# Optimization experiments

Hardware: AMD Instinct MI355X
Metric: run time of the kernel (lower is better)

The kernel has to match this reference:

```python
import jax, jax.numpy as jnp
import numpy as np

H, L, N1, N2, N3 = 256, 141, 9, 34, 98
B, S = 64, 512

def setup_inputs() -> dict:
    key = jax.random.key(0)
    cnt = [0]
    def nrm(shape, s=0.05):
        cnt[0] += 1
        return jax.random.normal(jax.random.fold_in(key, cnt[0]), shape, jnp.float32) * s
    d = {}
    d['inputs'] = jax.random.randint(jax.random.fold_in(key, 1000), (B, S), 0, 30522)
    d['text_hidden'] = nrm((B, S, 768), 1.0)
    d['label_encoding'] = nrm((L, H), 1.0)
    d['w12'] = (jax.random.uniform(jax.random.fold_in(key, 1001), (N1, N2)) < 0.3).astype(jnp.float32)
    d['w23'] = (jax.random.uniform(jax.random.fold_in(key, 1002), (N2, N3)) < 0.3).astype(jnp.float32)
    d['fre12'] = jax.random.uniform(jax.random.fold_in(key, 1003), (N1, N2), jnp.float32)
    d['fre23'] = jax.random.uniform(jax.random.fold_in(key, 1004), (N2, N3), jnp.float32)
    for name in ['wi1', 'wf1', 'wo1', 'wu1', 'wi2', 'wf2', 'wo2', 'wu2']:
        d[name + '_W'] = nrm((H, H)); d[name + '_b'] = nrm((H,))
    for name in ['ui1', 'uf1', 'uo1', 'uu1', 'ui2', 'uf2', 'uo2', 'uu2']:
        d[name + '_W'] = nrm((H, H))
    d['mix_W'] = nrm((3 * H, H)); d['mix_b'] = nrm((H,))
    d['tt_W'] = nrm((768, H)); d['tt_b'] = nrm((H,))
    d['A'] = nrm((L, L)); d['Wp'] = nrm((H, H))
    d['out_W'] = nrm((L * H, L)); d['out_b'] = nrm((L,))
    return d

def reference(inputs, text_hidden, label_encoding, w12, w23, fre12, fre23,
              wi1_W, wi1_b, wf1_W, wf1_b, wo1_W, wo1_b, wu1_W, wu1_b,
              wi2_W, wi2_b, wf2_W, wf2_b, wo2_W, wo2_b, wu2_W, wu2_b,
              ui1_W, uf1_W, uo1_W, uu1_W, ui2_W, uf2_W, uo2_W, uu2_W,
              mix_W, mix_b, tt_W, tt_b, A, Wp, out_W, out_b):
    sig, tanh = jax.nn.sigmoid, jnp.tanh
    v1 = label_encoding[:N1]          # [N1,H]
    v2 = label_encoding[N1:N1 + N2]   # [N2,H]
    v3 = label_encoding[N1 + N2:]     # [N3,H]
    w21, w32 = w12.T, w23.T
    # --- top-down tree-LSTM (suffix 1) ---
    i11 = sig(v1 @ wi1_W + wi1_b); o11 = sig(v1 @ wo1_W + wo1_b); u11 = tanh(v1 @ wu1_W + wu1_b)
    c11 = i11 * u11; h11 = o11 * tanh(c11)
    h21t = w21 @ h11
    i21 = sig(v2 @ wi1_W + wi1_b + h21t @ ui1_W)
    f21 = sig(v2 @ wf1_W + wf1_b + h21t @ uf1_W)
    o21 = sig(v2 @ wo1_W + wo1_b + h21t @ uo1_W)
    u21 = tanh(v2 @ wu1_W + wu1_b + h21t @ uu1_W)
    c21 = i21 * u21 + f21 * (w21 @ c11); h21 = o21 * tanh(c21)
    h31t = w32 @ h21
    i31 = sig(v3 @ wi1_W + wi1_b + h31t @ ui1_W)
    f31 = sig(v3 @ wf1_W + wf1_b + h31t @ uf1_W)
    o31 = sig(v3 @ wo1_W + wo1_b + h31t @ uo1_W)
    u31 = tanh(v3 @ wu1_W + wu1_b + h31t @ uu1_W)
    c31 = i31 * u31 + f31 * (w32 @ c21); h31 = o31 * tanh(c31)
    # --- bottom-up tree-LSTM (suffix 2) ---
    i32 = sig(v3 @ wi2_W + wi2_b); o32 = sig(v3 @ wo2_W + wo2_b); u32 = tanh(v3 @ wu2_W + wu2_b)
    c32 = i32 * u32; h32 = o32 * tanh(c32)
    h22t = fre23 @ h32
    i22 = sig(v2 @ wi2_W + wi2_b + h22t @ ui2_W)
    f22 = sig((w32 @ v2) @ wf2_W + wf2_b + h32 @ uf2_W)   # [N3,H]
    o22 = sig(v2 @ wo2_W + wo2_b + h22t @ uo2_W)
    u22 = tanh(v2 @ wu2_W + wu2_b + h22t @ uu2_W)
    c22 = i22 * u22 + w23 @ (f22 * c32); h22 = o22 * tanh(c22)
    h12t = fre12 @ h22
    i12 = sig(v1 @ wi2_W + wi2_b + h12t @ ui2_W)
    f12 = sig((w21 @ v1) @ wf2_W + wf2_b + h22 @ uf2_W)   # [N2,H]
    o12 = sig(v1 @ wo2_W + wo2_b + h12t @ uo2_W)
    u12 = tanh(v1 @ wu2_W + wu2_b + h12t @ uu2_W)
    c12 = i12 * u12 + w12 @ (f12 * c22); h12 = o12 * tanh(c12)
    h1 = jnp.concatenate([h11, h12], axis=1)
    h2 = jnp.concatenate([h21, h22], axis=1)
    h3 = jnp.concatenate([h31, h32], axis=1)
    le = jnp.concatenate([h1, h2, h3], axis=0)            # [L,2H]
    temp = jax.nn.relu(A @ label_encoding @ Wp)           # [L,H]
    le = jnp.concatenate([le, temp], axis=1) @ mix_W + mix_b  # [L,H]
    # --- masked cross-attention pooling over text ---
    text = tanh(text_hidden @ tt_W + tt_b)                # [B,S,H]
    att = jnp.einsum('lh,bsh->bls', le, text)             # [B,L,S]
    pad = jnp.where((inputs == 0) | (inputs == 101) | (inputs == 102), -jnp.inf, 0.0).astype(text.dtype)
    att = jax.nn.softmax(att + pad[:, None, :], axis=2)
    features = jnp.einsum('bls,bsh->blh', att, text).reshape(inputs.shape[0], -1)  # [B,L*H]
    return sig(features @ out_W + out_b)                  # [B,L]
```

## Files before the change

kernel.cpp:

```cpp
#include <hip/hip_runtime.h>
#include <math.h>

static constexpr int H = 256, L = 141, N1 = 9, N2 = 34, N3 = 98;
static constexpr int B = 64, S = 512;

typedef __attribute__((ext_vector_type(8))) _Float16 f16x8;
typedef __attribute__((ext_vector_type(4))) float f32x4;

__device__ inline unsigned short f2h(float x) {
    _Float16 h = (_Float16)x;
    return __builtin_bit_cast(unsigned short, h);
}
__device__ inline float sigf(float x) { return 1.f / (1.f + __expf(-x)); }

__device__ inline void gload_lds16(const void* g, void* l) {
    __builtin_amdgcn_global_load_lds(
        (const __attribute__((address_space(1))) void*)g,
        (__attribute__((address_space(3))) void*)l, 16, 0, 0);
}

__global__ __launch_bounds__(256) void conv_ttW(
    const float* __restrict__ W, unsigned short* __restrict__ Bt)
{
    __shared__ unsigned short Tl[32][257];
    const int t = blockIdx.x, tid = threadIdx.x;
    #pragma unroll
    for (int p = 0; p < 32; p++) {
        int lin = p * 256 + tid;
        int r = lin >> 8, c = lin & 255;
        Tl[r][c] = f2h(W[(long)(t * 32 + r) * 256 + c]);
    }
    __syncthreads();
    unsigned short v[32];
    #pragma unroll
    for (int kin = 0; kin < 32; kin++) v[kin] = Tl[kin][tid];
    uint4* dst = (uint4*)(Bt + ((long)t * 256 + tid) * 32);
    #pragma unroll
    for (int q = 0; q < 4; q++) dst[q] = ((const uint4*)v)[q];
}

__global__ __launch_bounds__(512, 4) void text_gemm3(
    const float* __restrict__ Af,
    const unsigned short* __restrict__ Bt,
    const float* __restrict__ bias,
    unsigned short* __restrict__ outH,
    unsigned short* __restrict__ outHT)
{
    __shared__ unsigned short smem[28672];
    unsigned short* As = smem;
    unsigned short* Bs = smem + 4096;
    unsigned short* T  = smem;

    const int tid  = threadIdx.x;
    const int wave = tid >> 6, lane = tid & 63;
    const int quad = lane >> 4, l16 = lane & 15;
    const int m0 = blockIdx.x * 64;
    const int wm = (wave >> 2) * 32;
    const int wn = (wave & 3) * 64;

    const int arow = tid >> 3;
    const int ac16 = tid & 7;
    const float* aSrc = Af + (long)(m0 + arow) * 768 + ac16 * 4;
    const int ac8d = ac16 ^ ((arow & 3) << 1);
    const int aWoff = arow * 32 + ac8d * 4;

    const int bsc = (lane & 3) ^ ((lane >> 3) & 3);
    const long bSrcOff0 = (long)(wave * 32 + (lane >> 2)) * 32 + bsc * 8;
    const long bSrcOff1 = bSrcOff0 + 16 * 32;
    const int bDst0 = (wave * 32) * 32, bDst1 = (wave * 32 + 16) * 32;

    int aro[2], bro[4];
    #pragma unroll
    for (int i = 0; i < 2; i++) {
        int r = wm + i * 16 + l16;
        aro[i] = r * 32 + ((quad * 2) ^ ((r & 3) << 1)) * 4;
    }
    #pragma unroll
    for (int j = 0; j < 4; j++) {
        int n = wn + j * 16 + l16;
        bro[j] = n * 32 + ((quad ^ ((n >> 1) & 3)) << 3);
    }

    f32x4 acc[2][4] = {};
    float4 ar0, ar1;

    auto issueB = [&](int kt, int pb) {
        const unsigned short* src = Bt + (long)kt * 8192;
        unsigned short* d = Bs + pb * 8192;
        gload_lds16(src + bSrcOff0, d + bDst0);
        gload_lds16(src + bSrcOff1, d + bDst1);
    };
    auto writeA = [&](const float4& v, int pa) {
        unsigned int p0 = f2h(v.x) | ((unsigned int)f2h(v.y) << 16);
        unsigned int p1 = f2h(v.z) | ((unsigned int)f2h(v.w) << 16);
        *(uint2*)&As[pa * 2048 + aWoff] = make_uint2(p0, p1);
    };

    ar0 = *(const float4*)(aSrc + 0 * 32);
    issueB(0, 0);
    ar1 = *(const float4*)(aSrc + 1 * 32);
    issueB(1, 1);
    asm volatile("s_waitcnt vmcnt(5)" ::: "memory");
    writeA(ar0, 0);
    asm volatile("s_waitcnt vmcnt(3)" ::: "memory");
    asm volatile("s_waitcnt lgkmcnt(0)" ::: "memory");
    asm volatile("s_barrier" ::: "memory");

    auto body = [&](int t, float4& arIn, float4& arOut, int pa, int pr) {
        int kt2 = (t + 2 <= 23) ? t + 2 : 23;
        arOut = *(const float4*)(aSrc + kt2 * 32);
        f16x8 a[2], b[4];
        const unsigned short* ab = As + pa * 2048;
        const unsigned short* bb = Bs + pr * 8192;
        #pragma unroll
        for (int i = 0; i < 2; i++) a[i] = *(const f16x8*)&ab[aro[i]];
        #pragma unroll
        for (int j = 0; j < 4; j++) b[j] = *(const f16x8*)&bb[bro[j]];
        #pragma unroll
        for (int i = 0; i < 2; i++)
            #pragma unroll
            for (int j = 0; j < 4; j++)
                acc[i][j] = __builtin_amdgcn_mfma_f32_16x16x32_f16(
                    a[i], b[j], acc[i][j], 0, 0, 0);
        asm volatile("s_waitcnt vmcnt(3)" ::: "memory");
        writeA(arIn, pa ^ 1);
        int pw = pr + 2; if (pw >= 3) pw -= 3;
        issueB(kt2, pw);
        asm volatile("s_waitcnt vmcnt(3)" ::: "memory");
        asm volatile("s_waitcnt lgkmcnt(0)" ::: "memory");
        asm volatile("s_barrier" ::: "memory");
    };

    int pr = 0;
    #pragma unroll 1
    for (int t = 0; t < 24; t += 2) {
        body(t,     ar1, ar0, t & 1 ? 1 : 0, pr);
        int pr1 = pr + 1; if (pr1 >= 3) pr1 -= 3;
        body(t + 1, ar0, ar1, 1, pr1);
        pr = pr1 + 1; if (pr >= 3) pr -= 3;
    }
    asm volatile("s_waitcnt vmcnt(0)" ::: "memory");
    __syncthreads();

    float bv[4];
    #pragma unroll
    for (int j = 0; j < 4; j++) bv[j] = bias[wn + j * 16 + l16];

    #pragma unroll
    for (int i = 0; i < 2; i++) {
        #pragma unroll
        for (int j = 0; j < 4; j++) {
            const int mlb = wm + i * 16 + quad * 4;
            const int n   = wn + j * 16 + l16;
            unsigned short hv[4];
            #pragma unroll
            for (int r = 0; r < 4; r++) {
                float v = tanhf(acc[i][j][r] + bv[j]);
                hv[r] = f2h(v);
                outH[(long)(m0 + mlb + r) * 256 + n] = hv[r];
            }
            uint2 p;
            p.x = hv[0] | ((unsigned int)hv[1] << 16);
            p.y = hv[2] | ((unsigned int)hv[3] << 16);
            *(uint2*)&T[n * 72 + mlb] = p;
        }
    }
    __syncthreads();
    {
        const int bb2 = m0 >> 9, s0 = m0 & 511;
        const int n = tid >> 1, half = tid & 1;
        const uint4* src = (const uint4*)&T[n * 72 + half * 32];
        uint4* dst = (uint4*)&outHT[((long)bb2 * 256 + n) * 512 + s0 + half * 32];
        dst[0] = src[0]; dst[1] = src[1];
        dst[2] = src[2]; dst[3] = src[3];
    }
}

__global__ __launch_bounds__(512, 4) void att_logits(
    const unsigned short* __restrict__ le_h,
    const unsigned short* __restrict__ text_h,
    const int* __restrict__ tokens,
    float* __restrict__ att)
{
    __shared__ unsigned short A_s[64 * 256];
    __shared__ unsigned short Bs[3][256 * 32];
    const int tid  = threadIdx.x;
    const int wave = tid >> 6, lane = tid & 63;
    const int quad = lane >> 4, l16 = lane & 15;
    const int s0 = blockIdx.x * 256;
    const int m0 = blockIdx.y * 64;
    const int b  = blockIdx.z;
    const int wm = (wave >> 2) * 32;
    const int wn = (wave & 3) * 64;

    const int bsc = (lane & 3) ^ ((lane >> 3) & 3);
    const long bOff0 = (long)(b * 512 + s0 + wave * 32 + (lane >> 2)) * 256 + bsc * 8;
    const long bOff1 = bOff0 + 16 * 256;
    const int bDst0 = (wave * 32) * 32, bDst1 = bDst0 + 16 * 32;
    auto issueB = [&](int kt, int pb) {
        gload_lds16(text_h + bOff0 + kt * 32, &Bs[pb][bDst0]);
        gload_lds16(text_h + bOff1 + kt * 32, &Bs[pb][bDst1]);
    };

    int abase[2], axm[2], bro[4];
    #pragma unroll
    for (int i = 0; i < 2; i++) {
        int r = wm + i * 16 + l16;
        abase[i] = r * 256; axm[i] = r & 7;
    }
    #pragma unroll
    for (int j = 0; j < 4; j++) {
        int n = wn + j * 16 + l16;
        bro[j] = n * 32 + ((quad ^ ((n >> 1) & 3)) << 3);
    }

    #pragma unroll
    for (int p = 0; p < 4; p++) {
        int row = p * 16 + (tid >> 5);
        int c   = tid & 31;
        int grow = m0 + row; if (grow > L - 1) grow = L - 1;
        gload_lds16(le_h + (long)grow * 256 + ((c ^ (row & 7)) << 3),
                    A_s + p * 4096 + wave * 512);
    }
    issueB(0, 0);
    issueB(1, 1);
    asm volatile("s_waitcnt vmcnt(2)" ::: "memory");
    asm volatile("s_barrier" ::: "memory");

    f32x4 acc[2][4] = {};
    #pragma unroll 1
    for (int t = 0; t < 8; t++) {
        const int pr = t % 3;
        f16x8 a[2], b[4];
        #pragma unroll
        for (int i = 0; i < 2; i++)
            a[i] = *(const f16x8*)&A_s[abase[i] + (((t * 4 + quad) ^ axm[i]) << 3)];
        const unsigned short* bb = &Bs[pr][0];
        #pragma unroll
        for (int j = 0; j < 4; j++) b[j] = *(const f16x8*)&bb[bro[j]];
        #pragma unroll
        for (int i = 0; i < 2; i++)
            #pragma unroll
            for (int j = 0; j < 4; j++)
                acc[i][j] = __builtin_amdgcn_mfma_f32_16x16x32_f16(
                    a[i], b[j], acc[i][j], 0, 0, 0);
        if (t < 7) {
            int kt2 = (t + 2 <= 7) ? t + 2 : 7;
            int pw = (t + 2) % 3;
            issueB(kt2, pw);
            asm volatile("s_waitcnt vmcnt(2)" ::: "memory");
            asm volatile("s_barrier" ::: "memory");
        }
    }
    asm volatile("s_waitcnt vmcnt(0)" ::: "memory");

    float mvv[4];
    #pragma unroll
    for (int j = 0; j < 4; j++) {
        int gs = s0 + wn + j * 16 + l16;
        int tok = tokens[(long)b * 512 + gs];
        mvv[j] = (tok == 0 || tok == 101 || tok == 102) ? 1e30f : 0.f;
    }
    #pragma unroll
    for (int i = 0; i < 2; i++)
        #pragma unroll
        for (int j = 0; j < 4; j++)
            #pragma unroll
            for (int r = 0; r < 4; r++) {
                int gm = m0 + wm + i * 16 + quad * 4 + r;
                if (gm < L) {
                    int gs = s0 + wn + j * 16 + l16;
                    att[(long)b * (L * S) + (long)gm * 512 + gs] =
                        acc[i][j][r] - mvv[j];
                }
            }
}

__global__ __launch_bounds__(512, 4) void att_pv(
    const unsigned short* __restrict__ att_h,
    const unsigned short* __restrict__ text_hT,
    unsigned short* __restrict__ feat_h)
{
    __shared__ unsigned short As[2 * 64 * 64];
    __shared__ unsigned short Bs[3][256 * 32];
    const int tid  = threadIdx.x;
    const int wave = tid >> 6, lane = tid & 63;
    const int quad = lane >> 4, l16 = lane & 15;
    const int m0 = blockIdx.x * 64;
    const int b  = blockIdx.y;
    const int wm = (wave >> 2) * 32;
    const int wn = (wave & 3) * 64;

    int arow = m0 + wave * 8 + (lane >> 3); if (arow > L - 1) arow = L - 1;
    const int asc = (lane & 7) ^ (lane >> 3);
    const unsigned short* aSrc = att_h + ((long)b * L + arow) * 512 + asc * 8;
    const int aDst = wave * 512;
    auto issueA = [&](int ka, int pa) {
        gload_lds16(aSrc + ka * 64, &As[pa * 4096 + aDst]);
    };

    const int bsc = (lane & 3) ^ ((lane >> 3) & 3);
    const long bOff0 = ((long)b * 256 + wave * 32 + (lane >> 2)) * 512 + bsc * 8;
    const long bOff1 = bOff0 + 16 * 512;
    const int bDst0 = (wave * 32) * 32, bDst1 = bDst0 + 16 * 32;
    auto issueB = [&](int kt, int pb) {
        gload_lds16(text_hT + bOff0 + kt * 32, &Bs[pb][bDst0]);
        gload_lds16(text_hT + bOff1 + kt * 32, &Bs[pb][bDst1]);
    };

    int aro[2], axm[2], bro[4];
    #pragma unroll
    for (int i = 0; i < 2; i++) {
        int r = wm + i * 16 + l16;
        aro[i] = r * 64; axm[i] = r & 7;
    }
    #pragma unroll
    for (int j = 0; j < 4; j++) {
        int n = wn + j * 16 + l16;
        bro[j] = n * 32 + ((quad ^ ((n >> 1) & 3)) << 3);
    }

    issueA(0, 0);
    issueB(0, 0);
    issueB(1, 1);
    asm volatile("s_waitcnt vmcnt(2)" ::: "memory");
    asm volatile("s_barrier" ::: "memory");

    f32x4 acc[2][4] = {};
    #pragma unroll 1
    for (int t = 0; t < 16; t++) {
        const int pa = (t >> 1) & 1, pr = t % 3, sub = t & 1;
        f16x8 a[2], bfr[4];
        const unsigned short* ab = &As[pa * 4096];
        #pragma unroll
        for (int i = 0; i < 2; i++)
            a[i] = *(const f16x8*)&ab[aro[i] + (((sub * 4 + quad) ^ axm[i]) << 3)];
        const unsigned short* bb = &Bs[pr][0];
        #pragma unroll
        for (int j = 0; j < 4; j++) bfr[j] = *(const f16x8*)&bb[bro[j]];
        #pragma unroll
        for (int i = 0; i < 2; i++)
            #pragma unroll
            for (int j = 0; j < 4; j++)
                acc[i][j] = __builtin_amdgcn_mfma_f32_16x16x32_f16(
                    a[i], bfr[j], acc[i][j], 0, 0, 0);
        if (t < 15) {
            if (sub == 0) {
                int ka = (t >> 1) + 1; if (ka > 7) ka = 7;
                issueA(ka, pa ^ 1);
            }
            int kb = t + 2; if (kb > 15) kb = 15;
            issueB(kb, (t + 2) % 3);
            if (sub == 0) {
                asm volatile("s_waitcnt vmcnt(3)" ::: "memory");
            } else {
                asm volatile("s_waitcnt vmcnt(2)" ::: "memory");
            }
            asm volatile("s_barrier" ::: "memory");
        }
    }
    asm volatile("s_waitcnt vmcnt(0)" ::: "memory");

    #pragma unroll
    for (int i = 0; i < 2; i++)
        #pragma unroll
        for (int j = 0; j < 4; j++)
            #pragma unroll
            for (int r = 0; r < 4; r++) {
                int gm = m0 + wm + i * 16 + quad * 4 + r;
                if (gm < L) {
                    int h = wn + j * 16 + l16;
                    feat_h[(long)b * (L * H) + (long)gm * 256 + h] =
                        f2h(acc[i][j][r]);
                }
            }
}

template<int EPI, bool CONVA, int IM>
__global__ __launch_bounds__(256) void gemm_mfma(
    const void* __restrict__ Aptr, int lda, long strA,
    const unsigned short* __restrict__ Bp, int ldb, long strB,
    float* __restrict__ C, int ldc, long strC,
    int M, int N, int K,
    const float* __restrict__ bias,
    const int* __restrict__ tokens,
    unsigned short* __restrict__ outH,
    unsigned short* __restrict__ outHT,
    int kChunk)
{
    __shared__ unsigned short A_s[32 * IM * 32];
    __shared__ unsigned short B_s[128 * 32];
    const int tid  = threadIdx.x;
    const int wave = tid >> 6, lane = tid & 63;
    const int quad = lane >> 4, l16 = lane & 15;
    const int bz = blockIdx.z;
    const int m0 = blockIdx.y * (32 * IM), n0 = blockIdx.x * 128;
    const int wm = (wave & 1) * (16 * IM), wn = (wave >> 1) * 64;

    long aBase, bBase;
    int kBeg, kEnd;
    if (EPI == 4) { aBase = 0; bBase = 0; kBeg = bz * kChunk; kEnd = kBeg + kChunk; }
    else { aBase = (long)bz * strA; bBase = (long)bz * strB; kBeg = 0; kEnd = K; }

    f32x4 acc[IM][4] = {};

    for (int k0 = kBeg; k0 < kEnd; k0 += 32) {
        if (CONVA) {
            const float* Af = (const float*)Aptr + aBase;
            #pragma unroll
            for (int it = 0; it < IM; it++) {
                int idx = it * 256 + tid;
                int row = idx >> 3, col4 = idx & 7;
                int gm = m0 + row; if (gm > M - 1) gm = M - 1;
                float4 v = *(const float4*)(Af + (long)gm * lda + k0 + col4 * 4);
                unsigned int p0 = f2h(v.x) | ((unsigned int)f2h(v.y) << 16);
                unsigned int p1 = f2h(v.z) | ((unsigned int)f2h(v.w) << 16);
                *(uint2*)&A_s[row * 32 + col4 * 4] = make_uint2(p0, p1);
            }
        } else {
            const unsigned short* Ab = (const unsigned short*)Aptr + aBase;
            #pragma unroll
            for (int t = 0; t < IM / 2; t++) {
                int rowb = wave * (8 * IM) + t * 16;
                int gm = m0 + rowb + (lane >> 2); if (gm > M - 1) gm = M - 1;
                gload_lds16(Ab + (long)gm * lda + k0 + (lane & 3) * 8,
                            &A_s[rowb * 32]);
            }
        }
        #pragma unroll
        for (int t = 0; t < 2; t++) {
            int rowb = wave * 32 + t * 16;
            int gn = n0 + rowb + (lane >> 2); if (gn > N - 1) gn = N - 1;
            gload_lds16(Bp + bBase + (long)gn * ldb + k0 + (lane & 3) * 8,
                        &B_s[rowb * 32]);
        }
        __syncthreads();
        f16x8 a[IM], b[4];
        #pragma unroll
        for (int i = 0; i < IM; i++)
            a[i] = *(const f16x8*)&A_s[(wm + i * 16 + l16) * 32 + quad * 8];
        #pragma unroll
        for (int j = 0; j < 4; j++)
            b[j] = *(const f16x8*)&B_s[(wn + j * 16 + l16) * 32 + quad * 8];
        #pragma unroll
        for (int i = 0; i < IM; i++)
            #pragma unroll
            for (int j = 0; j < 4; j++)
                acc[i][j] = __builtin_amdgcn_mfma_f32_16x16x32_f16(
                    a[i], b[j], acc[i][j], 0, 0, 0);
        __syncthreads();
    }

    #pragma unroll
    for (int i = 0; i < IM; i++) {
        #pragma unroll
        for (int j = 0; j < 4; j++) {
            #pragma unroll
            for (int r = 0; r < 4; r++) {
                int ml = wm + i * 16 + quad * 4 + r;
                int nl = wn + j * 16 + l16;
                int gm = m0 + ml, gn = n0 + nl;
                if (gm >= M || gn >= N) continue;
                float v = acc[i][j][r];
                if (EPI == 2) {
                    int tok = tokens[(long)bz * 512 + gn];
                    if (tok == 0 || tok == 101 || tok == 102) v -= 1e30f;
                    C[(long)bz * strC + (long)gm * ldc + gn] = v;
                } else if (EPI == 3) {
                    outH[(long)bz * strC + (long)gm * ldc + gn] = f2h(v);
                } else {
                    C[(long)bz * strC + (long)gm * ldc + gn] = v;
                }
            }
        }
    }
}

__global__ __launch_bounds__(256) void transp_t64(
    const float* __restrict__ src, unsigned short* __restrict__ dst,
    int R, int C)
{
    __shared__ unsigned short T[64 * 65];
    const int tid = threadIdx.x;
    const int r0 = blockIdx.x * 64, c0 = blockIdx.y * 64;
    #pragma unroll
    for (int p = 0; p < 16; p++) {
        int lin = p * 256 + tid;
        int r = lin >> 6, c = lin & 63;
        int gc = c0 + c;
        float v = (gc < C) ? src[(long)(r0 + r) * C + gc] : 0.f;
        T[c * 65 + r] = f2h(v);
    }
    __syncthreads();
    #pragma unroll
    for (int p = 0; p < 16; p++) {
        int lin = p * 256 + tid;
        int c = lin >> 6, r = lin & 63;
        if (c0 + c < C)
            dst[(long)(c0 + c) * R + r0 + r] = T[c * 65 + r];
    }
}

__global__ __launch_bounds__(256) void gate_pre(
    const float* __restrict__ le,
    const float* W0, const float* W1, const float* W2, const float* W3,
    const float* W4, const float* W5, const float* W6,
    const float* b0, const float* b1, const float* b2, const float* b3,
    const float* b4, const float* b5, const float* b6,
    float* __restrict__ G)
{
    __shared__ float ls[256];
    __shared__ float red[256];
    const int j = blockIdx.x >> 2, x = blockIdx.x & 3, m = blockIdx.y;
    const int tid = threadIdx.x, nl = tid & 63, ks = tid >> 6, n = x * 64 + nl;
    ls[tid] = le[(long)m * 256 + tid];
    __syncthreads();
    const float *W, *bb;
    switch (j) {
        case 0: W = W0; bb = b0; break;  case 1: W = W1; bb = b1; break;
        case 2: W = W2; bb = b2; break;  case 3: W = W3; bb = b3; break;
        case 4: W = W4; bb = b4; break;  case 5: W = W5; bb = b5; break;
        default: W = W6; bb = b6;
    }
    float a0 = 0, a1 = 0, a2 = 0, a3 = 0;
    for (int k = ks; k + 12 < 256; k += 16) {
        long o = (long)k * 256 + n;
        a0 += ls[k] * W[o];        a1 += ls[k + 4] * W[o + 1024];
        a2 += ls[k + 8] * W[o + 2048]; a3 += ls[k + 12] * W[o + 3072];
    }
    red[tid] = a0 + a1 + a2 + a3;
    __syncthreads();
    if (ks == 0)
        G[((long)j * 141 + m) * 256 + n] =
            red[nl] + red[64 + nl] + red[128 + nl] + red[192 + nl] + bb[n];
}

__global__ __launch_bounds__(256) void pre2(
    const float* __restrict__ A, const float* __restrict__ le,
    const float* __restrict__ w23, const float* __restrict__ w12,
    const float* __restrict__ Wp, const float* __restrict__ wf2_W,
    float* __restrict__ tmpP, float* __restrict__ wv2f, float* __restrict__ wv1f)
{
    __shared__ float cs[141];
    __shared__ float t[256];
    __shared__ float red[256];
    const int x = blockIdx.x, y = blockIdx.y;
    const int tid = threadIdx.x, nl = tid & 63, ks = tid >> 6, n = x * 64 + nl;
    int job, m, K1;
    if (y < 141)      { job = 0; m = y;       K1 = 141; }
    else if (y < 239) { job = 1; m = y - 141; K1 = 34; }
    else              { job = 2; m = y - 239; K1 = 9; }
    if (tid < K1)
        cs[tid] = (job == 0) ? A[(long)m * 141 + tid]
                : (job == 1) ? w23[(long)tid * 98 + m]
                             : w12[(long)tid * 34 + m];
    __syncthreads();
    const float* s1 = (job == 1) ? le + 9 * 256 : le;
    float acc = 0;
    #pragma unroll 4
    for (int k = 0; k < K1; k++) acc += cs[k] * s1[(long)k * 256 + tid];
    t[tid] = acc;
    __syncthreads();
    const float* W = (job == 0) ? Wp : wf2_W;
    float a0 = 0, a1 = 0, a2 = 0, a3 = 0;
    for (int k = ks; k + 12 < 256; k += 16) {
        long o = (long)k * 256 + n;
        a0 += t[k] * W[o];        a1 += t[k + 4] * W[o + 1024];
        a2 += t[k + 8] * W[o + 2048]; a3 += t[k + 12] * W[o + 3072];
    }
    red[tid] = a0 + a1 + a2 + a3;
    __syncthreads();
    if (ks == 0) {
        float tot = red[nl] + red[64 + nl] + red[128 + nl] + red[192 + nl];
        if (job == 0)      tmpP[(long)m * 256 + n] = fmaxf(tot, 0.f);
        else if (job == 1) wv2f[(long)m * 256 + n] = tot;
        else               wv1f[(long)m * 256 + n] = tot;
    }
}

__global__ __launch_bounds__(256) void ew1(
    const float* __restrict__ G, float* __restrict__ h11, float* __restrict__ c11,
    float* __restrict__ h32, float* __restrict__ c32)
{
    int y = blockIdx.x, n = threadIdx.x;
    if (y < 9) {
        int m = y;
        float iv = sigf(G[(0L * 141 + m) * 256 + n]);
        float ov = sigf(G[(2L * 141 + m) * 256 + n]);
        float uv = tanhf(G[(3L * 141 + m) * 256 + n]);
        float cv = iv * uv;
        c11[m * 256 + n] = cv; h11[m * 256 + n] = ov * tanhf(cv);
    } else {
        int r = y - 9, grow = 43 + r;
        float iv = sigf(G[(4L * 141 + grow) * 256 + n]);
        float ov = sigf(G[(5L * 141 + grow) * 256 + n]);
        float uv = tanhf(G[(6L * 141 + grow) * 256 + n]);
        float cv = iv * uv;
        c32[r * 256 + n] = cv; h32[r * 256 + n] = ov * tanhf(cv);
    }
}

__global__ __launch_bounds__(256) void chain_mm(int phase,
    const float* __restrict__ w12, const float* __restrict__ w23,
    const float* __restrict__ fre23, const float* __restrict__ fre12,
    const float* __restrict__ h11, const float* __restrict__ c11,
    const float* __restrict__ h32,
    const float* __restrict__ h21, const float* __restrict__ c21,
    const float* __restrict__ h22,
    const float* __restrict__ wv2f, const float* __restrict__ wv1f,
    const float* __restrict__ wf2_b, const float* __restrict__ uf2_W,
    const float* __restrict__ c32, const float* __restrict__ c22,
    float* __restrict__ h21t, float* __restrict__ c21p,
    float* __restrict__ h22t, float* __restrict__ fcb,
    float* __restrict__ h31t, float* __restrict__ c31p,
    float* __restrict__ h12t, float* __restrict__ fc2b)
{
    __shared__ float cs[256];
    __shared__ float red[256];
    const int x = blockIdx.x, y = blockIdx.y;
    const int tid = threadIdx.x, nl = tid & 63, ks = tid >> 6, n = x * 64 + nl;
    int job, m;
    if (phase == 0) {
        if (y < 34)       { job = 0; m = y; }
        else if (y < 68)  { job = 1; m = y - 34; }
        else if (y < 102) { job = 2; m = y - 68; }
        else              { job = 3; m = y - 102; }
    } else {
        if (y < 98)       { job = 0; m = y; }
        else if (y < 196) { job = 1; m = y - 98; }
        else if (y < 205) { job = 2; m = y - 196; }
        else              { job = 3; m = y - 205; }
    }
    if (job < 3) {
        int K; const float* src; float* dst;
        if (phase == 0) {
            K = (job == 2) ? 98 : 9;
            src = (job == 0) ? h11 : (job == 1) ? c11 : h32;
            dst = (job == 0) ? h21t : (job == 1) ? c21p : h22t;
            if (tid < K)
                cs[tid] = (job == 2) ? fre23[(long)m * 98 + tid]
                                     : w12[(long)tid * 34 + m];
        } else {
            K = 34;
            src = (job == 0) ? h21 : (job == 1) ? c21 : h22;
            dst = (job == 0) ? h31t : (job == 1) ? c31p : h12t;
            if (tid < K)
                cs[tid] = (job == 2) ? fre12[(long)m * 34 + tid]
                                     : w23[(long)tid * 98 + m];
        }
        __syncthreads();
        float a0 = 0;
        for (int k = ks; k < K; k += 4) a0 += cs[k] * src[(long)k * 256 + n];
        red[tid] = a0;
        __syncthreads();
        if (ks == 0)
            dst[(long)m * 256 + n] = red[nl] + red[64 + nl] + red[128 + nl] + red[192 + nl];
    } else {
        const float* row = (phase == 0) ? h32 + m * 256 : h22 + m * 256;
        const float* pre = (phase == 0) ? wv2f : wv1f;
        const float* cm  = (phase == 0) ? c32 : c22;
        float* dst       = (phase == 0) ? fcb : fc2b;
        cs[tid] = row[tid];
        __syncthreads();
        float a0 = 0, a1 = 0, a2 = 0, a3 = 0;
        for (int k = ks; k + 12 < 256; k += 16) {
            long o = (long)k * 256 + n;
            a0 += cs[k] * uf2_W[o];        a1 += cs[k + 4] * uf2_W[o + 1024];
            a2 += cs[k + 8] * uf2_W[o + 2048]; a3 += cs[k + 12] * uf2_W[o + 3072];
        }
        red[tid] = a0 + a1 + a2 + a3;
        __syncthreads();
        if (ks == 0) {
            float tot = red[nl] + red[64 + nl] + red[128 + nl] + red[192 + nl]
                      + pre[(long)m * 256 + n] + wf2_b[n];
            dst[(long)m * 256 + n] = sigf(tot) * cm[(long)m * 256 + n];
        }
    }
}

__global__ __launch_bounds__(256) void lstm_fused(int phase,
    const float* __restrict__ G,
    const float* __restrict__ h21t, const float* __restrict__ c21p,
    const float* __restrict__ h22t, const float* __restrict__ fcb,
    const float* __restrict__ h31t, const float* __restrict__ c31p,
    const float* __restrict__ h12t, const float* __restrict__ fc2b,
    const float* __restrict__ w23, const float* __restrict__ w12,
    const float* __restrict__ ui1, const float* __restrict__ uf1,
    const float* __restrict__ uo1, const float* __restrict__ uu1,
    const float* __restrict__ ui2, const float* __restrict__ uo2,
    const float* __restrict__ uu2,
    float* __restrict__ h21, float* __restrict__ c21,
    float* __restrict__ h22, float* __restrict__ c22,
    float* __restrict__ h31, float* __restrict__ h12)
{
    __shared__ float hs[256];
    __shared__ float cs[128];
    __shared__ float red[1024];
    const int x = blockIdx.x, y = blockIdx.y;
    const int tid = threadIdx.x, nl = tid & 63, ks = tid >> 6, n = x * 64 + nl;
    bool modef; int m, grow, Kx = 0;
    const float *hrow, *U0, *U1, *U2, *U3 = nullptr, *Sx = nullptr, *cmod = nullptr;
    float *ho, *co = nullptr;
    if (phase == 0) {
        if (y < 34) { modef = true;  m = y;      grow = 9 + m;  hrow = h21t;
                      U0 = ui1; U1 = uf1; U2 = uo1; U3 = uu1; cmod = c21p; ho = h21; co = c21; }
        else        { modef = false; m = y - 34; grow = 9 + m;  hrow = h22t;
                      U0 = ui2; U1 = uo2; U2 = uu2; Sx = fcb; Kx = 98; ho = h22; co = c22;
                      if (tid < 98) cs[tid] = w23[(long)m * 98 + tid]; }
    } else {
        if (y < 98) { modef = true;  m = y;      grow = 43 + m; hrow = h31t;
                      U0 = ui1; U1 = uf1; U2 = uo1; U3 = uu1; cmod = c31p; ho = h31; co = nullptr; }
        else        { modef = false; m = y - 98; grow = m;      hrow = h12t;
                      U0 = ui2; U1 = uo2; U2 = uu2; Sx = fc2b; Kx = 34; ho = h12; co = nullptr;
                      if (tid < 34) cs[tid] = w12[(long)m * 34 + tid]; }
    }
    hs[tid] = hrow[(long)m * 256 + tid];
    __syncthreads();
    float a0 = 0, a1 = 0, a2 = 0, a3 = 0;
    if (modef) {
        for (int k = ks; k < 256; k += 4) {
            float xv = hs[k]; long o = (long)k * 256 + n;
            a0 += xv * U0[o]; a1 += xv * U1[o]; a2 += xv * U2[o]; a3 += xv * U3[o];
        }
    } else {
        for (int k = ks; k < 256; k += 4) {
            float xv = hs[k]; long o = (long)k * 256 + n;
            a0 += xv * U0[o]; a1 += xv * U1[o]; a2 += xv * U2[o];
        }
        for (int k = ks; k < Kx; k += 4) a3 += cs[k] * Sx[(long)k * 256 + n];
    }
    red[tid] = a0; red[256 + tid] = a1; red[512 + tid] = a2; red[768 + tid] = a3;
    __syncthreads();
    if (ks == 0) {
        float t0 = 0, t1 = 0, t2 = 0, t3 = 0;
        #pragma unroll
        for (int s2 = 0; s2 < 4; s2++) {
            t0 += red[s2 * 64 + nl];       t1 += red[256 + s2 * 64 + nl];
            t2 += red[512 + s2 * 64 + nl]; t3 += red[768 + s2 * 64 + nl];
        }
        if (modef) {
            float ti = t0 + G[(0L * 141 + grow) * 256 + n];
            float tf = t1 + G[(1L * 141 + grow) * 256 + n];
            float to = t2 + G[(2L * 141 + grow) * 256 + n];
            float tu = t3 + G[(3L * 141 + grow) * 256 + n];
            float cv = sigf(ti) * tanhf(tu) + sigf(tf) * cmod[(long)m * 256 + n];
            ho[(long)m * 256 + n] = sigf(to) * tanhf(cv);
            if (co) co[(long)m * 256 + n] = cv;
        } else {
            float ti = t0 + G[(4L * 141 + grow) * 256 + n];
            float to = t1 + G[(5L * 141 + grow) * 256 + n];
            float tu = t2 + G[(6L * 141 + grow) * 256 + n];
            float cv = sigf(ti) * tanhf(tu) + t3;
            ho[(long)m * 256 + n] = sigf(to) * tanhf(cv);
            if (co) co[(long)m * 256 + n] = cv;
        }
    }
}

__global__ __launch_bounds__(256) void mix_mm(
    const float* __restrict__ h11, const float* __restrict__ h12,
    const float* __restrict__ h21, const float* __restrict__ h22,
    const float* __restrict__ h31, const float* __restrict__ h32,
    const float* __restrict__ tmpP, const float* __restrict__ mix_W,
    const float* __restrict__ mix_b, unsigned short* __restrict__ le_h)
{
    __shared__ float ls[768];
    __shared__ float red[256];
    const int x = blockIdx.x, l = blockIdx.y;
    const int tid = threadIdx.x, nl = tid & 63, ks = tid >> 6, n = x * 64 + nl;
    const float *pa, *pb; int r;
    if (l < 9)       { pa = h11; pb = h12; r = l; }
    else if (l < 43) { pa = h21; pb = h22; r = l - 9; }
    else             { pa = h31; pb = h32; r = l - 43; }
    for (int j = tid; j < 768; j += 256) {
        float v;
        if (j < 256)      v = pa[r * 256 + j];
        else if (j < 512) v = pb[r * 256 + (j - 256)];
        else              v = tmpP[l * 256 + (j - 512)];
        ls[j] = v;
    }
    __syncthreads();
    float a0 = 0, a1 = 0, a2 = 0, a3 = 0;
    for (int k = ks; k + 12 < 768; k += 16) {
        long o = (long)k * 256 + n;
        a0 += ls[k] * mix_W[o];        a1 += ls[k + 4] * mix_W[o + 1024];
        a2 += ls[k + 8] * mix_W[o + 2048]; a3 += ls[k + 12] * mix_W[o + 3072];
    }
    red[tid] = a0 + a1 + a2 + a3;
    __syncthreads();
    if (ks == 0) {
        float tot = red[nl] + red[64 + nl] + red[128 + nl] + red[192 + nl] + mix_b[n];
        le_h[(long)l * 256 + n] = f2h(tot);
    }
}

__global__ __launch_bounds__(256) void softmax512(
    const float* __restrict__ att, unsigned short* __restrict__ atth)
{
    __shared__ float red[256];
    const float* row = att + (long)blockIdx.x * 512;
    unsigned short* orow = atth + (long)blockIdx.x * 512;
    int t = threadIdx.x;
    float a = row[t], b = row[t + 256];
    red[t] = fmaxf(a, b);
    __syncthreads();
    for (int s = 128; s > 0; s >>= 1) {
        if (t < s) red[t] = fmaxf(red[t], red[t + s]);
        __syncthreads();
    }
    float m = red[0];
    __syncthreads();
    float ea = __expf(a - m), eb = __expf(b - m);
    red[t] = ea + eb;
    __syncthreads();
    for (int s = 128; s > 0; s >>= 1) {
        if (t < s) red[t] += red[t + s];
        __syncthreads();
    }
    float inv = 1.f / red[0];
    orow[t] = f2h(ea * inv);
    orow[t + 256] = f2h(eb * inv);
}

__global__ __launch_bounds__(256) void out_final(
    const float* __restrict__ acc, const float* __restrict__ ob,
    float* __restrict__ out, int total, int nz)
{
    int i = blockIdx.x * 256 + threadIdx.x;
    if (i >= total) return;
    float v = ob[i % L];
    #pragma unroll 4
    for (int z = 0; z < nz; z++) v += acc[(long)z * total + i];
    out[i] = sigf(v);
}

extern "C" void kernel_launch(void* const* d_in, const int* in_sizes, int n_in,
                              void* d_out, int out_size, void* d_ws, size_t ws_size,
                              hipStream_t stream)
{
    (void)in_sizes; (void)n_in; (void)out_size; (void)ws_size;
    const int*   inputs      = (const int*)d_in[0];
    const float* text_hidden = (const float*)d_in[1];
    const float* label_enc   = (const float*)d_in[2];
    const float* w12   = (const float*)d_in[3];
    const float* w23   = (const float*)d_in[4];
    const float* fre12 = (const float*)d_in[5];
    const float* fre23 = (const float*)d_in[6];
    const float* wi1_W = (const float*)d_in[7],  *wi1_b = (const float*)d_in[8];
    const float* wf1_W = (const float*)d_in[9],  *wf1_b = (const float*)d_in[10];
    const float* wo1_W = (const float*)d_in[11], *wo1_b = (const float*)d_in[12];
    const float* wu1_W = (const float*)d_in[13], *wu1_b = (const float*)d_in[14];
    const float* wi2_W = (const float*)d_in[15], *wi2_b = (const float*)d_in[16];
    const float* wf2_W = (const float*)d_in[17], *wf2_b = (const float*)d_in[18];
    const float* wo2_W = (const float*)d_in[19], *wo2_b = (const float*)d_in[20];
    const float* wu2_W = (const float*)d_in[21], *wu2_b = (const float*)d_in[22];
    const float* ui1_W = (const float*)d_in[23], *uf1_W = (const float*)d_in[24];
    const float* uo1_W = (const float*)d_in[25], *uu1_W = (const float*)d_in[26];
    const float* ui2_W = (const float*)d_in[27], *uf2_W = (const float*)d_in[28];
    const float* uo2_W = (const float*)d_in[29], *uu2_W = (const float*)d_in[30];
    const float* mix_W = (const float*)d_in[31], *mix_b = (const float*)d_in[32];
    const float* tt_W  = (const float*)d_in[33], *tt_b  = (const float*)d_in[34];
    const float* Amat  = (const float*)d_in[35], *Wp    = (const float*)d_in[36];
    const float* out_W = (const float*)d_in[37], *out_b = (const float*)d_in[38];
    float* out = (float*)d_out;

    float* ws = (float*)d_ws;
    float* att     = ws; ws += (long)B * L * S;
    unsigned short* text_h  = (unsigned short*)ws; ws += (long)B * S * H / 2;
    unsigned short* text_hT = (unsigned short*)ws; ws += (long)B * S * H / 2;
    unsigned short* att_h   = (unsigned short*)ws; ws += (long)B * L * S / 2;
    unsigned short* tt_Wt   = (unsigned short*)ws; ws += 768 * H / 2;
    unsigned short* le_h    = (unsigned short*)ws; ws += L * H / 2 + 4;
    unsigned short* out_Wh  = (unsigned short*)ws; ws += (long)L * 36096 / 2;
    unsigned short* feat_h  = (unsigned short*)ws; ws += (long)B * L * H / 2;
    float* outacc = ws; ws += (long)B * L * 141;
    float* G    = ws; ws += 7 * 141 * 256;
    float* tmpP = ws; ws += L * H;
    float* wv2f = ws; ws += N3 * H;
    float* wv1f = ws; ws += N2 * H;
    float* h11  = ws; ws += N1 * H;  float* c11  = ws; ws += N1 * H;
    float* h21  = ws; ws += N2 * H;  float* c21  = ws; ws += N2 * H;
    float* h21t = ws; ws += N2 * H;  float* c21p = ws; ws += N2 * H;
    float* h31  = ws; ws += N3 * H;  float* h31t = ws; ws += N3 * H;
    float* c31p = ws; ws += N3 * H;
    float* h32  = ws; ws += N3 * H;  float* c32  = ws; ws += N3 * H;
    float* h22  = ws; ws += N2 * H;  float* c22  = ws; ws += N2 * H;
    float* h22t = ws; ws += N2 * H;  float* fcb  = ws; ws += N3 * H;
    float* h12  = ws; ws += N1 * H;  float* h12t = ws; ws += N1 * H;
    float* fc2b = ws; ws += N2 * H;

    conv_ttW<<<24, 256, 0, stream>>>(tt_W, tt_Wt);
    text_gemm3<<<512, 512, 0, stream>>>(
        text_hidden, tt_Wt, tt_b, text_h, text_hT);
    gate_pre<<<dim3(28, 141), 256, 0, stream>>>(label_enc,
        wi1_W, wf1_W, wo1_W, wu1_W, wi2_W, wo2_W, wu2_W,
        wi1_b, wf1_b, wo1_b, wu1_b, wi2_b, wo2_b, wu2_b, G);
    pre2<<<dim3(4, 273), 256, 0, stream>>>(Amat, label_enc, w23, w12, Wp, wf2_W,
        tmpP, wv2f, wv1f);
    transp_t64<<<dim3(36096 / 64, 3), 256, 0, stream>>>(out_W, out_Wh, 36096, 141);
    ew1<<<107, 256, 0, stream>>>(G, h11, c11, h32, c32);
    chain_mm<<<dim3(4, 200), 256, 0, stream>>>(0, w12, w23, fre23, fre12,
        h11, c11, h32, h21, c21, h22, wv2f, wv1f, wf2_b, uf2_W, c32, c22,
        h21t, c21p, h22t, fcb, h31t, c31p, h12t, fc2b);
    lstm_fused<<<dim3(4, 68), 256, 0, stream>>>(0, G,
        h21t, c21p, h22t, fcb, h31t, c31p, h12t, fc2b, w23, w12,
        ui1_W, uf1_W, uo1_W, uu1_W, ui2_W, uo2_W, uu2_W,
        h21, c21, h22, c22, h31, h12);
    chain_mm<<<dim3(4, 239), 256, 0, stream>>>(1, w12, w23, fre23, fre12,
        h11, c11, h32, h21, c21, h22, wv2f, wv1f, wf2_b, uf2_W, c32, c22,
        h21t, c21p, h22t, fcb, h31t, c31p, h12t, fc2b);
    lstm_fused<<<dim3(4, 107), 256, 0, stream>>>(1, G,
        h21t, c21p, h22t, fcb, h31t, c31p, h12t, fc2b, w23, w12,
        ui1_W, uf1_W, uo1_W, uu1_W, ui2_W, uo2_W, uu2_W,
        h21, c21, h22, c22, h31, h12);
    mix_mm<<<dim3(4, 141), 256, 0, stream>>>(h11, h12, h21, h22, h31, h32,
        tmpP, mix_W, mix_b, le_h);
    att_logits<<<dim3(2, 3, 64), 512, 0, stream>>>(
        le_h, text_h, inputs, att);
    softmax512<<<B * L, 256, 0, stream>>>(att, att_h);
    att_pv<<<dim3(3, 64), 512, 0, stream>>>(att_h, text_hT, feat_h);
    gemm_mfma<4, false, 2><<<dim3(2, 1, 141), 256, 0, stream>>>(
        feat_h, L * H, 0, out_Wh, L * H, 0, outacc, L, (long)B * L,
        B, L, L * H, nullptr, nullptr, nullptr, nullptr, 256);
    out_final<<<(B * L + 255) / 256, 256, 0, stream>>>(outacc, out_b, out, B * L, 141);
}
```

Measured before the change: 454.0 us.

## Fuse softmax into attention logits kernel and merge small prep launches

Replaces the separate att_logits + softmax512 pair with a single att_logits2 kernel that computes logits across the full sequence per block and writes normalized fp16 attention directly. This drops the fp32 att round trip through global memory and one launch. It also merges conv_ttW with the out_W transpose, and gate_pre with pre2, into single launches to cut launch overhead. The cost is a lower grid count for the logits kernel (3x64 blocks instead of 2x3x64), which may reduce occupancy.

```diff
diff --git a/kernel.cpp b/kernel.cpp
--- a/kernel.cpp
+++ b/kernel.cpp
@@ -19,24 +19,49 @@
         (__attribute__((address_space(3))) void*)l, 16, 0, 0);
 }
 
-__global__ __launch_bounds__(256) void conv_ttW(
-    const float* __restrict__ W, unsigned short* __restrict__ Bt)
+__global__ __launch_bounds__(256) void prep(
+    const float* __restrict__ ttW, unsigned short* __restrict__ Bt,
+    const float* __restrict__ outW, unsigned short* __restrict__ outWh)
 {
     __shared__ unsigned short Tl[32][257];
-    const int t = blockIdx.x, tid = threadIdx.x;
-    #pragma unroll
-    for (int p = 0; p < 32; p++) {
-        int lin = p * 256 + tid;
-        int r = lin >> 8, c = lin & 255;
-        Tl[r][c] = f2h(W[(long)(t * 32 + r) * 256 + c]);
-    }
-    __syncthreads();
-    unsigned short v[32];
-    #pragma unroll
-    for (int kin = 0; kin < 32; kin++) v[kin] = Tl[kin][tid];
-    uint4* dst = (uint4*)(Bt + ((long)t * 256 + tid) * 32);
-    #pragma unroll
-    for (int q = 0; q < 4; q++) dst[q] = ((const uint4*)v)[q];
+    __shared__ unsigned short T2[64 * 65];
+    const int tid = threadIdx.x;
+    if (blockIdx.x < 24) {
+        const int t = blockIdx.x;
+        #pragma unroll
+        for (int p = 0; p < 32; p++) {
+            int lin = p * 256 + tid;
+            int r = lin >> 8, c = lin & 255;
+            Tl[r][c] = f2h(ttW[(long)(t * 32 + r) * 256 + c]);
+        }
+        __syncthreads();
+        unsigned short v[32];
+        #pragma unroll
+        for (int kin = 0; kin < 32; kin++) v[kin] = Tl[kin][tid];
+        uint4* dst = (uint4*)(Bt + ((long)t * 256 + tid) * 32);
+        #pragma unroll
+        for (int q = 0; q < 4; q++) dst[q] = ((const uint4*)v)[q];
+    } else {
+        const int u = blockIdx.x - 24;
+        const int r0 = (u % 564) * 64, c0 = (u / 564) * 64;
+        const int R = 36096, C = 141;
+        #pragma unroll
+        for (int p = 0; p < 16; p++) {
+            int lin = p * 256 + tid;
+            int r = lin >> 6, c = lin & 63;
+            int gc = c0 + c;
+            float v = (gc < C) ? outW[(long)(r0 + r) * C + gc] : 0.f;
+            T2[c * 65 + r] = f2h(v);
+        }
+        __syncthreads();
+        #pragma unroll
+        for (int p = 0; p < 16; p++) {
+            int lin = p * 256 + tid;
+            int c = lin >> 6, r = lin & 63;
+            if (c0 + c < C)
+                outWh[(long)(c0 + c) * R + r0 + r] = T2[c * 65 + r];
+        }
+    }
 }
 
 __global__ __launch_bounds__(512, 4) void text_gemm3(
@@ -176,405 +201,80 @@
     }
 }
 
-__global__ __launch_bounds__(512, 4) void att_logits(
-    const unsigned short* __restrict__ le_h,
-    const unsigned short* __restrict__ text_h,
-    const int* __restrict__ tokens,
-    float* __restrict__ att)
-{
-    __shared__ unsigned short A_s[64 * 256];
-    __shared__ unsigned short Bs[3][256 * 32];
-    const int tid  = threadIdx.x;
-    const int wave = tid >> 6, lane = tid & 63;
-    const int quad = lane >> 4, l16 = lane & 15;
-    const int s0 = blockIdx.x * 256;
-    const int m0 = blockIdx.y * 64;
-    const int b  = blockIdx.z;
-    const int wm = (wave >> 2) * 32;
-    const int wn = (wave & 3) * 64;
-
-    const int bsc = (lane & 3) ^ ((lane >> 3) & 3);
-    const long bOff0 = (long)(b * 512 + s0 + wave * 32 + (lane >> 2)) * 256 + bsc * 8;
-    const long bOff1 = bOff0 + 16 * 256;
-    const int bDst0 = (wave * 32) * 32, bDst1 = bDst0 + 16 * 32;
-    auto issueB = [&](int kt, int pb) {
-        gload_lds16(text_h + bOff0 + kt * 32, &Bs[pb][bDst0]);
-        gload_lds16(text_h + bOff1 + kt * 32, &Bs[pb][bDst1]);
-    };
-
-    int abase[2], axm[2], bro[4];
-    #pragma unroll
-    for (int i = 0; i < 2; i++) {
-        int r = wm + i * 16 + l16;
-        abase[i] = r * 256; axm[i] = r & 7;
-    }
-    #pragma unroll
-    for (int j = 0; j < 4; j++) {
-        int n = wn + j * 16 + l16;
-        bro[j] = n * 32 + ((quad ^ ((n >> 1) & 3)) << 3);
-    }
-
-    #pragma unroll
-    for (int p = 0; p < 4; p++) {
-        int row = p * 16 + (tid >> 5);
-        int c   = tid & 31;
-        int grow = m0 + row; if (grow > L - 1) grow = L - 1;
-        gload_lds16(le_h + (long)grow * 256 + ((c ^ (row & 7)) << 3),
-                    A_s + p * 4096 + wave * 512);
-    }
-    issueB(0, 0);
-    issueB(1, 1);
-    asm volatile("s_waitcnt vmcnt(2)" ::: "memory");
-    asm volatile("s_barrier" ::: "memory");
-
-    f32x4 acc[2][4] = {};
-    #pragma unroll 1
-    for (int t = 0; t < 8; t++) {
-        const int pr = t % 3;
-        f16x8 a[2], b[4];
-        #pragma unroll
-        for (int i = 0; i < 2; i++)
-            a[i] = *(const f16x8*)&A_s[abase[i] + (((t * 4 + quad) ^ axm[i]) << 3)];
-        const unsigned short* bb = &Bs[pr][0];
-        #pragma unroll
-        for (int j = 0; j < 4; j++) b[j] = *(const f16x8*)&bb[bro[j]];
-        #pragma unroll
-        for (int i = 0; i < 2; i++)
-            #pragma unroll
-            for (int j = 0; j < 4; j++)
-                acc[i][j] = __builtin_amdgcn_mfma_f32_16x16x32_f16(
-                    a[i], b[j], acc[i][j], 0, 0, 0);
-        if (t < 7) {
-            int kt2 = (t + 2 <= 7) ? t + 2 : 7;
-            int pw = (t + 2) % 3;
-            issueB(kt2, pw);
-            asm volatile("s_waitcnt vmcnt(2)" ::: "memory");
-            asm volatile("s_barrier" ::: "memory");
-        }
-    }
-    asm volatile("s_waitcnt vmcnt(0)" ::: "memory");
-
-    float mvv[4];
-    #pragma unroll
-    for (int j = 0; j < 4; j++) {
-        int gs = s0 + wn + j * 16 + l16;
-        int tok = tokens[(long)b * 512 + gs];
-        mvv[j] = (tok == 0 || tok == 101 || tok == 102) ? 1e30f : 0.f;
-    }
-    #pragma unroll
-    for (int i = 0; i < 2; i++)
-        #pragma unroll
-        for (int j = 0; j < 4; j++)
-            #pragma unroll
-            for (int r = 0; r < 4; r++) {
-                int gm = m0 + wm + i * 16 + quad * 4 + r;
-                if (gm < L) {
-                    int gs = s0 + wn + j * 16 + l16;
-                    att[(long)b * (L * S) + (long)gm * 512 + gs] =
-                        acc[i][j][r] - mvv[j];
-                }
-            }
-}
-
-__global__ __launch_bounds__(512, 4) void att_pv(
-    const unsigned short* __restrict__ att_h,
-    const unsigned short* __restrict__ text_hT,
-    unsigned short* __restrict__ feat_h)
-{
-    __shared__ unsigned short As[2 * 64 * 64];
-    __shared__ unsigned short Bs[3][256 * 32];
-    const int tid  = threadIdx.x;
-    const int wave = tid >> 6, lane = tid & 63;
-    const int quad = lane >> 4, l16 = lane & 15;
-    const int m0 = blockIdx.x * 64;
-    const int b  = blockIdx.y;
-    const int wm = (wave >> 2) * 32;
-    const int wn = (wave & 3) * 64;
-
-    int arow = m0 + wave * 8 + (lane >> 3); if (arow > L - 1) arow = L - 1;
-    const int asc = (lane & 7) ^ (lane >> 3);
-    const unsigned short* aSrc = att_h + ((long)b * L + arow) * 512 + asc * 8;
-    const int aDst = wave * 512;
-    auto issueA = [&](int ka, int pa) {
-        gload_lds16(aSrc + ka * 64, &As[pa * 4096 + aDst]);
-    };
-
-    const int bsc = (lane & 3) ^ ((lane >> 3) & 3);
-    const long bOff0 = ((long)b * 256 + wave * 32 + (lane >> 2)) * 512 + bsc * 8;
-    const long bOff1 = bOff0 + 16 * 512;
-    const int bDst0 = (wave * 32) * 32, bDst1 = bDst0 + 16 * 32;
-    auto issueB = [&](int kt, int pb) {
-        gload_lds16(text_hT + bOff0 + kt * 32, &Bs[pb][bDst0]);
-        gload_lds16(text_hT + bOff1 + kt * 32, &Bs[pb][bDst1]);
-    };
-
-    int aro[2], axm[2], bro[4];
-    #pragma unroll
-    for (int i = 0; i < 2; i++) {
-        int r = wm + i * 16 + l16;
-        aro[i] = r * 64; axm[i] = r & 7;
-    }
-    #pragma unroll
-    for (int j = 0; j < 4; j++) {
-        int n = wn + j * 16 + l16;
-        bro[j] = n * 32 + ((quad ^ ((n >> 1) & 3)) << 3);
-    }
-
-    issueA(0, 0);
-    issueB(0, 0);
-    issueB(1, 1);
-    asm volatile("s_waitcnt vmcnt(2)" ::: "memory");
-    asm volatile("s_barrier" ::: "memory");
-
-    f32x4 acc[2][4] = {};
-    #pragma unroll 1
-    for (int t = 0; t < 16; t++) {
-        const int pa = (t >> 1) & 1, pr = t % 3, sub = t & 1;
-        f16x8 a[2], bfr[4];
-        const unsigned short* ab = &As[pa * 4096];
-        #pragma unroll
-        for (int i = 0; i < 2; i++)
-            a[i] = *(const f16x8*)&ab[aro[i] + (((sub * 4 + quad) ^ axm[i]) << 3)];
-        const unsigned short* bb = &Bs[pr][0];
-        #pragma unroll
-        for (int j = 0; j < 4; j++) bfr[j] = *(const f16x8*)&bb[bro[j]];
-        #pragma unroll
-        for (int i = 0; i < 2; i++)
-            #pragma unroll
-            for (int j = 0; j < 4; j++)
-                acc[i][j] = __builtin_amdgcn_mfma_f32_16x16x32_f16(
-                    a[i], bfr[j], acc[i][j], 0, 0, 0);
-        if (t < 15) {
-            if (sub == 0) {
-                int ka = (t >> 1) + 1; if (ka > 7) ka = 7;
-                issueA(ka, pa ^ 1);
-            }
-            int kb = t + 2; if (kb > 15) kb = 15;
-            issueB(kb, (t + 2) % 3);
-            if (sub == 0) {
-                asm volatile("s_waitcnt vmcnt(3)" ::: "memory");
-            } else {
-                asm volatile("s_waitcnt vmcnt(2)" ::: "memory");
-            }
-            asm volatile("s_barrier" ::: "memory");
-        }
-    }
-    asm volatile("s_waitcnt vmcnt(0)" ::: "memory");
-
-    #pragma unroll
-    for (int i = 0; i < 2; i++)
-        #pragma unroll
-        for (int j = 0; j < 4; j++)
-            #pragma unroll
-            for (int r = 0; r < 4; r++) {
-                int gm = m0 + wm + i * 16 + quad * 4 + r;
-                if (gm < L) {
-                    int h = wn + j * 16 + l16;
-                    feat_h[(long)b * (L * H) + (long)gm * 256 + h] =
-                        f2h(acc[i][j][r]);
-                }
-            }
-}
-
-template<int EPI, bool CONVA, int IM>
-__global__ __launch_bounds__(256) void gemm_mfma(
-    const void* __restrict__ Aptr, int lda, long strA,
-    const unsigned short* __restrict__ Bp, int ldb, long strB,
-    float* __restrict__ C, int ldc, long strC,
-    int M, int N, int K,
-    const float* __restrict__ bias,
-    const int* __restrict__ tokens,
-    unsigned short* __restrict__ outH,
-    unsigned short* __restrict__ outHT,
-    int kChunk)
-{
-    __shared__ unsigned short A_s[32 * IM * 32];
-    __shared__ unsigned short B_s[128 * 32];
-    const int tid  = threadIdx.x;
-    const int wave = tid >> 6, lane = tid & 63;
-    const int quad = lane >> 4, l16 = lane & 15;
-    const int bz = blockIdx.z;
-    const int m0 = blockIdx.y * (32 * IM), n0 = blockIdx.x * 128;
-    const int wm = (wave & 1) * (16 * IM), wn = (wave >> 1) * 64;
-
-    long aBase, bBase;
-    int kBeg, kEnd;
-    if (EPI == 4) { aBase = 0; bBase = 0; kBeg = bz * kChunk; kEnd = kBeg + kChunk; }
-    else { aBase = (long)bz * strA; bBase = (long)bz * strB; kBeg = 0; kEnd = K; }
-
-    f32x4 acc[IM][4] = {};
-
-    for (int k0 = kBeg; k0 < kEnd; k0 += 32) {
-        if (CONVA) {
-            const float* Af = (const float*)Aptr + aBase;
-            #pragma unroll
-            for (int it = 0; it < IM; it++) {
-                int idx = it * 256 + tid;
-                int row = idx >> 3, col4 = idx & 7;
-                int gm = m0 + row; if (gm > M - 1) gm = M - 1;
-                float4 v = *(const float4*)(Af + (long)gm * lda + k0 + col4 * 4);
-                unsigned int p0 = f2h(v.x) | ((unsigned int)f2h(v.y) << 16);
-                unsigned int p1 = f2h(v.z) | ((unsigned int)f2h(v.w) << 16);
-                *(uint2*)&A_s[row * 32 + col4 * 4] = make_uint2(p0, p1);
-            }
-        } else {
-            const unsigned short* Ab = (const unsigned short*)Aptr + aBase;
-            #pragma unroll
-            for (int t = 0; t < IM / 2; t++) {
-                int rowb = wave * (8 * IM) + t * 16;
-                int gm = m0 + rowb + (lane >> 2); if (gm > M - 1) gm = M - 1;
-                gload_lds16(Ab + (long)gm * lda + k0 + (lane & 3) * 8,
-                            &A_s[rowb * 32]);
-            }
-        }
-        #pragma unroll
-        for (int t = 0; t < 2; t++) {
-            int rowb = wave * 32 + t * 16;
-            int gn = n0 + rowb + (lane >> 2); if (gn > N - 1) gn = N - 1;
-            gload_lds16(Bp + bBase + (long)gn * ldb + k0 + (lane & 3) * 8,
-                        &B_s[rowb * 32]);
-        }
-        __syncthreads();
-        f16x8 a[IM], b[4];
-        #pragma unroll
-        for (int i = 0; i < IM; i++)
-            a[i] = *(const f16x8*)&A_s[(wm + i * 16 + l16) * 32 + quad * 8];
-        #pragma unroll
-        for (int j = 0; j < 4; j++)
-            b[j] = *(const f16x8*)&B_s[(wn + j * 16 + l16) * 32 + quad * 8];
-        #pragma unroll
-        for (int i = 0; i < IM; i++)
-            #pragma unroll
-            for (int j = 0; j < 4; j++)
-                acc[i][j] = __builtin_amdgcn_mfma_f32_16x16x32_f16(
-                    a[i], b[j], acc[i][j], 0, 0, 0);
-        __syncthreads();
-    }
-
-    #pragma unroll
-    for (int i = 0; i < IM; i++) {
-        #pragma unroll
-        for (int j = 0; j < 4; j++) {
-            #pragma unroll
-            for (int r = 0; r < 4; r++) {
-                int ml = wm + i * 16 + quad * 4 + r;
-                int nl = wn + j * 16 + l16;
-                int gm = m0 + ml, gn = n0 + nl;
-                if (gm >= M || gn >= N) continue;
-                float v = acc[i][j][r];
-                if (EPI == 2) {
-                    int tok = tokens[(long)bz * 512 + gn];
-                    if (tok == 0 || tok == 101 || tok == 102) v -= 1e30f;
-                    C[(long)bz * strC + (long)gm * ldc + gn] = v;
-                } else if (EPI == 3) {
-                    outH[(long)bz * strC + (long)gm * ldc + gn] = f2h(v);
-                } else {
-                    C[(long)bz * strC + (long)gm * ldc + gn] = v;
-                }
-            }
-        }
-    }
-}
-
-__global__ __launch_bounds__(256) void transp_t64(
-    const float* __restrict__ src, unsigned short* __restrict__ dst,
-    int R, int C)
-{
-    __shared__ unsigned short T[64 * 65];
-    const int tid = threadIdx.x;
-    const int r0 = blockIdx.x * 64, c0 = blockIdx.y * 64;
-    #pragma unroll
-    for (int p = 0; p < 16; p++) {
-        int lin = p * 256 + tid;
-        int r = lin >> 6, c = lin & 63;
-        int gc = c0 + c;
-        float v = (gc < C) ? src[(long)(r0 + r) * C + gc] : 0.f;
-        T[c * 65 + r] = f2h(v);
-    }
-    __syncthreads();
-    #pragma unroll
-    for (int p = 0; p < 16; p++) {
-        int lin = p * 256 + tid;
-        int c = lin >> 6, r = lin & 63;
-        if (c0 + c < C)
-            dst[(long)(c0 + c) * R + r0 + r] = T[c * 65 + r];
-    }
-}
-
-__global__ __launch_bounds__(256) void gate_pre(
+__global__ __launch_bounds__(256) void gates_pre(
     const float* __restrict__ le,
     const float* W0, const float* W1, const float* W2, const float* W3,
     const float* W4, const float* W5, const float* W6,
     const float* b0, const float* b1, const float* b2, const float* b3,
     const float* b4, const float* b5, const float* b6,
-    float* __restrict__ G)
-{
-    __shared__ float ls[256];
-    __shared__ float red[256];
-    const int j = blockIdx.x >> 2, x = blockIdx.x & 3, m = blockIdx.y;
-    const int tid = threadIdx.x, nl = tid & 63, ks = tid >> 6, n = x * 64 + nl;
-    ls[tid] = le[(long)m * 256 + tid];
-    __syncthreads();
-    const float *W, *bb;
-    switch (j) {
-        case 0: W = W0; bb = b0; break;  case 1: W = W1; bb = b1; break;
-        case 2: W = W2; bb = b2; break;  case 3: W = W3; bb = b3; break;
-        case 4: W = W4; bb = b4; break;  case 5: W = W5; bb = b5; break;
-        default: W = W6; bb = b6;
-    }
-    float a0 = 0, a1 = 0, a2 = 0, a3 = 0;
-    for (int k = ks; k + 12 < 256; k += 16) {
-        long o = (long)k * 256 + n;
-        a0 += ls[k] * W[o];        a1 += ls[k + 4] * W[o + 1024];
-        a2 += ls[k + 8] * W[o + 2048]; a3 += ls[k + 12] * W[o + 3072];
-    }
-    red[tid] = a0 + a1 + a2 + a3;
-    __syncthreads();
-    if (ks == 0)
-        G[((long)j * 141 + m) * 256 + n] =
-            red[nl] + red[64 + nl] + red[128 + nl] + red[192 + nl] + bb[n];
-}
-
-__global__ __launch_bounds__(256) void pre2(
-    const float* __restrict__ A, const float* __restrict__ le,
-    const float* __restrict__ w23, const float* __restrict__ w12,
-    const float* __restrict__ Wp, const float* __restrict__ wf2_W,
-    float* __restrict__ tmpP, float* __restrict__ wv2f, float* __restrict__ wv1f)
-{
-    __shared__ float cs[141];
-    __shared__ float t[256];
-    __shared__ float red[256];
-    const int x = blockIdx.x, y = blockIdx.y;
-    const int tid = threadIdx.x, nl = tid & 63, ks = tid >> 6, n = x * 64 + nl;
-    int job, m, K1;
-    if (y < 141)      { job = 0; m = y;       K1 = 141; }
-    else if (y < 239) { job = 1; m = y - 141; K1 = 34; }
-    else              { job = 2; m = y - 239; K1 = 9; }
-    if (tid < K1)
-        cs[tid] = (job == 0) ? A[(long)m * 141 + tid]
-                : (job == 1) ? w23[(long)tid * 98 + m]
-                             : w12[(long)tid * 34 + m];
-    __syncthreads();
-    const float* s1 = (job == 1) ? le + 9 * 256 : le;
-    float acc = 0;
-    #pragma unroll 4
-    for (int k = 0; k < K1; k++) acc += cs[k] * s1[(long)k * 256 + tid];
-    t[tid] = acc;
-    __syncthreads();
-    const float* W = (job == 0) ? Wp : wf2_W;
-    float a0 = 0, a1 = 0, a2 = 0, a3 = 0;
-    for (int k = ks; k + 12 < 256; k += 16) {
-        long o = (long)k * 256 + n;
-        a0 += t[k] * W[o];        a1 += t[k + 4] * W[o + 1024];
-        a2 += t[k + 8] * W[o + 2048]; a3 += t[k + 12] * W[o + 3072];
-    }
-    red[tid] = a0 + a1 + a2 + a3;
-    __syncthreads();
-    if (ks == 0) {
-        float tot = red[nl] + red[64 + nl] + red[128 + nl] + red[192 + nl];
-        if (job == 0)      tmpP[(long)m * 256 + n] = fmaxf(tot, 0.f);
-        else if (job == 1) wv2f[(long)m * 256 + n] = tot;
-        else               wv1f[(long)m * 256 + n] = tot;
+    const float* __restrict__ Amat, const float* __restrict__ w23,
+    const float* __restrict__ w12, const float* __restrict__ Wp,
+    const float* __restrict__ wf2_W,
+    float* __restrict__ G, float* __restrict__ tmpP,
+    float* __restrict__ wv2f, float* __restrict__ wv1f)
+{
+    __shared__ float smem[768];
+    const int tid = threadIdx.x;
+    const int nl = tid & 63, ks = tid >> 6;
+    if (blockIdx.x < 28 * 141) {
+        const int u = blockIdx.x;
+        const int bx = u % 28, m = u / 28;
+        const int j = bx >> 2, x = bx & 3, n = x * 64 + nl;
+        float* ls = smem; float* red = smem + 256;
+        ls[tid] = le[(long)m * 256 + tid];
+        __syncthreads();
+        const float *W, *bb;
+        switch (j) {
+            case 0: W = W0; bb = b0; break;  case 1: W = W1; bb = b1; break;
+            case 2: W = W2; bb = b2; break;  case 3: W = W3; bb = b3; break;
+            case 4: W = W4; bb = b4; break;  case 5: W = W5; bb = b5; break;
+            default: W = W6; bb = b6;
+        }
+        float a0 = 0, a1 = 0, a2 = 0, a3 = 0;
+        for (int k = ks; k + 12 < 256; k += 16) {
+            long o = (long)k * 256 + n;
+            a0 += ls[k] * W[o];        a1 += ls[k + 4] * W[o + 1024];
+            a2 += ls[k + 8] * W[o + 2048]; a3 += ls[k + 12] * W[o + 3072];
+        }
+        red[tid] = a0 + a1 + a2 + a3;
+        __syncthreads();
+        if (ks == 0)
+            G[((long)j * 141 + m) * 256 + n] =
+                red[nl] + red[64 + nl] + red[128 + nl] + red[192 + nl] + bb[n];
+    } else {
+        const int u = blockIdx.x - 28 * 141;
+        const int x = u % 4, y = u / 4, n = x * 64 + nl;
+        int job, m, K1;
+        if (y < 141)      { job = 0; m = y;       K1 = 141; }
+        else if (y < 239) { job = 1; m = y - 141; K1 = 34; }
+        else              { job = 2; m = y - 239; K1 = 9; }
+        float* cs = smem; float* t = smem + 256; float* red = smem + 512;
+        if (tid < K1)
+            cs[tid] = (job == 0) ? Amat[(long)m * 141 + tid]
+                    : (job == 1) ? w23[(long)tid * 98 + m]
+                                 : w12[(long)tid * 34 + m];
+        __syncthreads();
+        const float* s1 = (job == 1) ? le + 9 * 256 : le;
+        float acc = 0;
+        #pragma unroll 4
+        for (int k = 0; k < K1; k++) acc += cs[k] * s1[(long)k * 256 + tid];
+        t[tid] = acc;
+        __syncthreads();
+        const float* W = (job == 0) ? Wp : wf2_W;
+        float a0 = 0, a1 = 0, a2 = 0, a3 = 0;
+        for (int k = ks; k + 12 < 256; k += 16) {
+            long o = (long)k * 256 + n;
+            a0 += t[k] * W[o];        a1 += t[k + 4] * W[o + 1024];
+            a2 += t[k + 8] * W[o + 2048]; a3 += t[k + 12] * W[o + 3072];
+        }
+        red[tid] = a0 + a1 + a2 + a3;
+        __syncthreads();
+        if (ks == 0) {
+            float tot = red[nl] + red[64 + nl] + red[128 + nl] + red[192 + nl];
+            if (job == 0)      tmpP[(long)m * 256 + n] = fmaxf(tot, 0.f);
+            else if (job == 1) wv2f[(long)m * 256 + n] = tot;
+            else               wv1f[(long)m * 256 + n] = tot;
+        }
     }
 }
 
@@ -794,32 +494,369 @@
     }
 }
 
-__global__ __launch_bounds__(256) void softmax512(
-    const float* __restrict__ att, unsigned short* __restrict__ atth)
-{
-    __shared__ float red[256];
-    const float* row = att + (long)blockIdx.x * 512;
-    unsigned short* orow = atth + (long)blockIdx.x * 512;
-    int t = threadIdx.x;
-    float a = row[t], b = row[t + 256];
-    red[t] = fmaxf(a, b);
+__global__ __launch_bounds__(512, 1) void att_logits2(
+    const unsigned short* __restrict__ le_h,
+    const unsigned short* __restrict__ text_h,
+    const int* __restrict__ tokens,
+    unsigned short* __restrict__ att_h)
+{
+    __shared__ unsigned short A_s[64 * 256];
+    __shared__ unsigned short Bs[2][512 * 32];
+    __shared__ float redm[8][32];
+    __shared__ float reds[8][32];
+    const int tid  = threadIdx.x;
+    const int wave = tid >> 6, lane = tid & 63;
+    const int quad = lane >> 4, l16 = lane & 15;
+    const int m0 = blockIdx.x * 64;
+    const int b  = blockIdx.y;
+    const int wm = (wave >> 2) * 32;
+    const int wn = (wave & 3) * 128;
+
+    const int bsc = (lane & 3) ^ ((lane >> 3) & 3);
+    const long bOffBase = (long)(b * 512 + wave * 64 + (lane >> 2)) * 256 + bsc * 8;
+    const int bDstBase = (wave * 64) * 32;
+    auto issueB = [&](int kt, int pb) {
+        #pragma unroll
+        for (int q = 0; q < 4; q++)
+            gload_lds16(text_h + bOffBase + (long)q * 16 * 256 + kt * 32,
+                        &Bs[pb][bDstBase + q * 16 * 32]);
+    };
+
+    int abase[2], axm[2], bro[8];
+    #pragma unroll
+    for (int i = 0; i < 2; i++) {
+        int r = wm + i * 16 + l16;
+        abase[i] = r * 256; axm[i] = r & 7;
+    }
+    #pragma unroll
+    for (int j = 0; j < 8; j++) {
+        int n = wn + j * 16 + l16;
+        bro[j] = n * 32 + ((quad ^ ((n >> 1) & 3)) << 3);
+    }
+
+    #pragma unroll
+    for (int p = 0; p < 4; p++) {
+        int row = p * 16 + (tid >> 5);
+        int c   = tid & 31;
+        int grow = m0 + row; if (grow > L - 1) grow = L - 1;
+        gload_lds16(le_h + (long)grow * 256 + ((c ^ (row & 7)) << 3),
+                    A_s + p * 4096 + wave * 512);
+    }
+    issueB(0, 0);
+    issueB(1, 1);
+    asm volatile("s_waitcnt vmcnt(4)" ::: "memory");
+    asm volatile("s_barrier" ::: "memory");
+
+    f32x4 acc[2][8] = {};
+    #pragma unroll 1
+    for (int t = 0; t < 8; t++) {
+        const int pb = t & 1;
+        f16x8 a[2], bf[8];
+        #pragma unroll
+        for (int i = 0; i < 2; i++)
+            a[i] = *(const f16x8*)&A_s[abase[i] + (((t * 4 + quad) ^ axm[i]) << 3)];
+        const unsigned short* bb = &Bs[pb][0];
+        #pragma unroll
+        for (int j = 0; j < 8; j++) bf[j] = *(const f16x8*)&bb[bro[j]];
+        #pragma unroll
+        for (int i = 0; i < 2; i++)
+            #pragma unroll
+            for (int j = 0; j < 8; j++)
+                acc[i][j] = __builtin_amdgcn_mfma_f32_16x16x32_f16(
+                    a[i], bf[j], acc[i][j], 0, 0, 0);
+        if (t < 7) {
+            asm volatile("s_waitcnt lgkmcnt(0)" ::: "memory");
+            asm volatile("s_barrier" ::: "memory");
+            int kt2 = (t + 2 <= 7) ? t + 2 : 7;
+            issueB(kt2, pb);
+            asm volatile("s_waitcnt vmcnt(4)" ::: "memory");
+            asm volatile("s_barrier" ::: "memory");
+        }
+    }
+    asm volatile("s_waitcnt vmcnt(0)" ::: "memory");
+
+    float mvv[8];
+    #pragma unroll
+    for (int j = 0; j < 8; j++) {
+        int gs = wn + j * 16 + l16;
+        int tok = tokens[(long)b * 512 + gs];
+        mvv[j] = (tok == 0 || tok == 101 || tok == 102) ? 1e30f : 0.f;
+    }
+    #pragma unroll
+    for (int i = 0; i < 2; i++)
+        #pragma unroll
+        for (int j = 0; j < 8; j++)
+            #pragma unroll
+            for (int r = 0; r < 4; r++) acc[i][j][r] -= mvv[j];
+
+    const int wgrp = (wave >> 2) * 4;
+    float M[2][4];
+    #pragma unroll
+    for (int i = 0; i < 2; i++)
+        #pragma unroll
+        for (int r = 0; r < 4; r++) {
+            float v = acc[i][0][r];
+            #pragma unroll
+            for (int j = 1; j < 8; j++) v = fmaxf(v, acc[i][j][r]);
+            #pragma unroll
+            for (int d = 1; d <= 8; d <<= 1) v = fmaxf(v, __shfl_xor(v, d));
+            if (l16 == 0) redm[wave][i * 16 + quad * 4 + r] = v;
+        }
     __syncthreads();
-    for (int s = 128; s > 0; s >>= 1) {
-        if (t < s) red[t] = fmaxf(red[t], red[t + s]);
-        __syncthreads();
-    }
-    float m = red[0];
+    #pragma unroll
+    for (int i = 0; i < 2; i++)
+        #pragma unroll
+        for (int r = 0; r < 4; r++) {
+            int rl = i * 16 + quad * 4 + r;
+            float v = redm[wgrp][rl];
+            #pragma unroll
+            for (int k = 1; k < 4; k++) v = fmaxf(v, redm[wgrp + k][rl]);
+            M[i][r] = v;
+        }
+
+    float psum[2][4] = {};
+    #pragma unroll
+    for (int i = 0; i < 2; i++)
+        #pragma unroll
+        for (int j = 0; j < 8; j++)
+            #pragma unroll
+            for (int r = 0; r < 4; r++) {
+                float e = __expf(acc[i][j][r] - M[i][r]);
+                acc[i][j][r] = e;
+                psum[i][r] += e;
+            }
+    #pragma unroll
+    for (int i = 0; i < 2; i++)
+        #pragma unroll
+        for (int r = 0; r < 4; r++) {
+            float v = psum[i][r];
+            #pragma unroll
+            for (int d = 1; d <= 8; d <<= 1) v += __shfl_xor(v, d);
+            if (l16 == 0) reds[wave][i * 16 + quad * 4 + r] = v;
+        }
     __syncthreads();
-    float ea = __expf(a - m), eb = __expf(b - m);
-    red[t] = ea + eb;
-    __syncthreads();
-    for (int s = 128; s > 0; s >>= 1) {
-        if (t < s) red[t] += red[t + s];
-        __syncthreads();
-    }
-    float inv = 1.f / red[0];
-    orow[t] = f2h(ea * inv);
-    orow[t + 256] = f2h(eb * inv);
+    #pragma unroll
+    for (int i = 0; i < 2; i++)
+        #pragma unroll
+        for (int r = 0; r < 4; r++) {
+            int rl = i * 16 + quad * 4 + r;
+            float s = reds[wgrp][rl] + reds[wgrp + 1][rl]
+                    + reds[wgrp + 2][rl] + reds[wgrp + 3][rl];
+            M[i][r] = 1.f / s;
+        }
+
+    #pragma unroll
+    for (int i = 0; i < 2; i++)
+        #pragma unroll
+        for (int r = 0; r < 4; r++) {
+            int gm = m0 + wm + i * 16 + quad * 4 + r;
+            if (gm < L) {
+                unsigned short* orow = att_h + ((long)b * L + gm) * 512;
+                #pragma unroll
+                for (int j = 0; j < 8; j++)
+                    orow[wn + j * 16 + l16] = f2h(acc[i][j][r] * M[i][r]);
+            }
+        }
+}
+
+__global__ __launch_bounds__(512, 4) void att_pv(
+    const unsigned short* __restrict__ att_h,
+    const unsigned short* __restrict__ text_hT,
+    unsigned short* __restrict__ feat_h)
+{
+    __shared__ unsigned short As[2 * 64 * 64];
+    __shared__ unsigned short Bs[3][256 * 32];
+    const int tid  = threadIdx.x;
+    const int wave = tid >> 6, lane = tid & 63;
+    const int quad = lane >> 4, l16 = lane & 15;
+    const int m0 = blockIdx.x * 64;
+    const int b  = blockIdx.y;
+    const int wm = (wave >> 2) * 32;
+    const int wn = (wave & 3) * 64;
+
+    int arow = m0 + wave * 8 + (lane >> 3); if (arow > L - 1) arow = L - 1;
+    const int asc = (lane & 7) ^ (lane >> 3);
+    const unsigned short* aSrc = att_h + ((long)b * L + arow) * 512 + asc * 8;
+    const int aDst = wave * 512;
+    auto issueA = [&](int ka, int pa) {
+        gload_lds16(aSrc + ka * 64, &As[pa * 4096 + aDst]);
+    };
+
+    const int bsc = (lane & 3) ^ ((lane >> 3) & 3);
+    const long bOff0 = ((long)b * 256 + wave * 32 + (lane >> 2)) * 512 + bsc * 8;
+    const long bOff1 = bOff0 + 16 * 512;
+    const int bDst0 = (wave * 32) * 32, bDst1 = bDst0 + 16 * 32;
+    auto issueB = [&](int kt, int pb) {
+        gload_lds16(text_hT + bOff0 + kt * 32, &Bs[pb][bDst0]);
+        gload_lds16(text_hT + bOff1 + kt * 32, &Bs[pb][bDst1]);
+    };
+
+    int aro[2], axm[2], bro[4];
+    #pragma unroll
+    for (int i = 0; i < 2; i++) {
+        int r = wm + i * 16 + l16;
+        aro[i] = r * 64; axm[i] = r & 7;
+    }
+    #pragma unroll
+    for (int j = 0; j < 4; j++) {
+        int n = wn + j * 16 + l16;
+        bro[j] = n * 32 + ((quad ^ ((n >> 1) & 3)) << 3);
+    }
+
+    issueA(0, 0);
+    issueB(0, 0);
+    issueB(1, 1);
+    asm volatile("s_waitcnt vmcnt(2)" ::: "memory");
+    asm volatile("s_barrier" ::: "memory");
+
+    f32x4 acc[2][4] = {};
+    #pragma unroll 1
+    for (int t = 0; t < 16; t++) {
+        const int pa = (t >> 1) & 1, pr = t % 3, sub = t & 1;
+        f16x8 a[2], bfr[4];
+        const unsigned short* ab = &As[pa * 4096];
+        #pragma unroll
+        for (int i = 0; i < 2; i++)
+            a[i] = *(const f16x8*)&ab[aro[i] + (((sub * 4 + quad) ^ axm[i]) << 3)];
+        const unsigned short* bb = &Bs[pr][0];
+        #pragma unroll
+        for (int j = 0; j < 4; j++) bfr[j] = *(const f16x8*)&bb[bro[j]];
+        #pragma unroll
+        for (int i = 0; i < 2; i++)
+            #pragma unroll
+            for (int j = 0; j < 4; j++)
+                acc[i][j] = __builtin_amdgcn_mfma_f32_16x16x32_f16(
+                    a[i], bfr[j], acc[i][j], 0, 0, 0);
+        if (t < 15) {
+            if (sub == 0) {
+                int ka = (t >> 1) + 1; if (ka > 7) ka = 7;
+                issueA(ka, pa ^ 1);
+            }
+            int kb = t + 2; if (kb > 15) kb = 15;
+            issueB(kb, (t + 2) % 3);
+            if (sub == 0) {
+                asm volatile("s_waitcnt vmcnt(3)" ::: "memory");
+            } else {
+                asm volatile("s_waitcnt vmcnt(2)" ::: "memory");
+            }
+            asm volatile("s_barrier" ::: "memory");
+        }
+    }
+    asm volatile("s_waitcnt vmcnt(0)" ::: "memory");
+
+    #pragma unroll
+    for (int i = 0; i < 2; i++)
+        #pragma unroll
+        for (int j = 0; j < 4; j++)
+            #pragma unroll
+            for (int r = 0; r < 4; r++) {
+                int gm = m0 + wm + i * 16 + quad * 4 + r;
+                if (gm < L) {
+                    int h = wn + j * 16 + l16;
+                    feat_h[(long)b * (L * H) + (long)gm * 256 + h] =
+                        f2h(acc[i][j][r]);
+                }
+            }
+}
+
+template<int EPI, bool CONVA, int IM>
+__global__ __launch_bounds__(256) void gemm_mfma(
+    const void* __restrict__ Aptr, int lda, long strA,
+    const unsigned short* __restrict__ Bp, int ldb, long strB,
+    float* __restrict__ C, int ldc, long strC,
+    int M, int N, int K,
+    const float* __restrict__ bias,
+    const int* __restrict__ tokens,
+    unsigned short* __restrict__ outH,
+    unsigned short* __restrict__ outHT,
+    int kChunk)
+{
+    __shared__ unsigned short A_s[32 * IM * 32];
+    __shared__ unsigned short B_s[128 * 32];
+    const int tid  = threadIdx.x;
+    const int wave = tid >> 6, lane = tid & 63;
+    const int quad = lane >> 4, l16 = lane & 15;
+    const int bz = blockIdx.z;
+    const int m0 = blockIdx.y * (32 * IM), n0 = blockIdx.x * 128;
+    const int wm = (wave & 1) * (16 * IM), wn = (wave >> 1) * 64;
+
+    long aBase, bBase;
+    int kBeg, kEnd;
+    if (EPI == 4) { aBase = 0; bBase = 0; kBeg = bz * kChunk; kEnd = kBeg + kChunk; }
+    else { aBase = (long)bz * strA; bBase = (long)bz * strB; kBeg = 0; kEnd = K; }
+
+    f32x4 acc[IM][4] = {};
+
+    for (int k0 = kBeg; k0 < kEnd; k0 += 32) {
+        if (CONVA) {
+            const float* Af = (const float*)Aptr + aBase;
+            #pragma unroll
+            for (int it = 0; it < IM; it++) {
+                int idx = it * 256 + tid;
+                int row = idx >> 3, col4 = idx & 7;
+                int gm = m0 + row; if (gm > M - 1) gm = M - 1;
+                float4 v = *(const float4*)(Af + (long)gm * lda + k0 + col4 * 4);
+                unsigned int p0 = f2h(v.x) | ((unsigned int)f2h(v.y) << 16);
+                unsigned int p1 = f2h(v.z) | ((unsigned int)f2h(v.w) << 16);
+                *(uint2*)&A_s[row * 32 + col4 * 4] = make_uint2(p0, p1);
+            }
+        } else {
+            const unsigned short* Ab = (const unsigned short*)Aptr + aBase;
+            #pragma unroll
+            for (int t = 0; t < IM / 2; t++) {
+                int rowb = wave * (8 * IM) + t * 16;
+                int gm = m0 + rowb + (lane >> 2); if (gm > M - 1) gm = M - 1;
+                gload_lds16(Ab + (long)gm * lda + k0 + (lane & 3) * 8,
+                            &A_s[rowb * 32]);
+            }
+        }
+        #pragma unroll
+        for (int t = 0; t < 2; t++) {
+            int rowb = wave * 32 + t * 16;
+            int gn = n0 + rowb + (lane >> 2); if (gn > N - 1) gn = N - 1;
+            gload_lds16(Bp + bBase + (long)gn * ldb + k0 + (lane & 3) * 8,
+                        &B_s[rowb * 32]);
+        }
+        __syncthreads();
+        f16x8 a[IM], b[4];
+        #pragma unroll
+        for (int i = 0; i < IM; i++)
+            a[i] = *(const f16x8*)&A_s[(wm + i * 16 + l16) * 32 + quad * 8];
+        #pragma unroll
+        for (int j = 0; j < 4; j++)
+            b[j] = *(const f16x8*)&B_s[(wn + j * 16 + l16) * 32 + quad * 8];
+        #pragma unroll
+        for (int i = 0; i < IM; i++)
+            #pragma unroll
+            for (int j = 0; j < 4; j++)
+                acc[i][j] = __builtin_amdgcn_mfma_f32_16x16x32_f16(
+                    a[i], b[j], acc[i][j], 0, 0, 0);
+        __syncthreads();
+    }
+
+    #pragma unroll
+    for (int i = 0; i < IM; i++) {
+        #pragma unroll
+        for (int j = 0; j < 4; j++) {
+            #pragma unroll
+            for (int r = 0; r < 4; r++) {
+                int ml = wm + i * 16 + quad * 4 + r;
+                int nl = wn + j * 16 + l16;
+                int gm = m0 + ml, gn = n0 + nl;
+                if (gm >= M || gn >= N) continue;
+                float v = acc[i][j][r];
+                if (EPI == 2) {
+                    int tok = tokens[(long)bz * 512 + gn];
+                    if (tok == 0 || tok == 101 || tok == 102) v -= 1e30f;
+                    C[(long)bz * strC + (long)gm * ldc + gn] = v;
+                } else if (EPI == 3) {
+                    outH[(long)bz * strC + (long)gm * ldc + gn] = f2h(v);
+                } else {
+                    C[(long)bz * strC + (long)gm * ldc + gn] = v;
+                }
+            }
+        }
+    }
 }
 
 __global__ __launch_bounds__(256) void out_final(
@@ -888,16 +925,15 @@
     float* h22t = ws; ws += N2 * H;  float* fcb  = ws; ws += N3 * H;
     float* h12  = ws; ws += N1 * H;  float* h12t = ws; ws += N1 * H;
     float* fc2b = ws; ws += N2 * H;
-
-    conv_ttW<<<24, 256, 0, stream>>>(tt_W, tt_Wt);
+    (void)att;
+
+    prep<<<24 + 564 * 3, 256, 0, stream>>>(tt_W, tt_Wt, out_W, out_Wh);
     text_gemm3<<<512, 512, 0, stream>>>(
         text_hidden, tt_Wt, tt_b, text_h, text_hT);
-    gate_pre<<<dim3(28, 141), 256, 0, stream>>>(label_enc,
+    gates_pre<<<28 * 141 + 4 * 273, 256, 0, stream>>>(label_enc,
         wi1_W, wf1_W, wo1_W, wu1_W, wi2_W, wo2_W, wu2_W,
-        wi1_b, wf1_b, wo1_b, wu1_b, wi2_b, wo2_b, wu2_b, G);
-    pre2<<<dim3(4, 273), 256, 0, stream>>>(Amat, label_enc, w23, w12, Wp, wf2_W,
-        tmpP, wv2f, wv1f);
-    transp_t64<<<dim3(36096 / 64, 3), 256, 0, stream>>>(out_W, out_Wh, 36096, 141);
+        wi1_b, wf1_b, wo1_b, wu1_b, wi2_b, wo2_b, wu2_b,
+        Amat, w23, w12, Wp, wf2_W, G, tmpP, wv2f, wv1f);
     ew1<<<107, 256, 0, stream>>>(G, h11, c11, h32, c32);
     chain_mm<<<dim3(4, 200), 256, 0, stream>>>(0, w12, w23, fre23, fre12,
         h11, c11, h32, h21, c21, h22, wv2f, wv1f, wf2_b, uf2_W, c32, c22,
@@ -915,9 +951,8 @@
         h21, c21, h22, c22, h31, h12);
     mix_mm<<<dim3(4, 141), 256, 0, stream>>>(h11, h12, h21, h22, h31, h32,
         tmpP, mix_W, mix_b, le_h);
-    att_logits<<<dim3(2, 3, 64), 512, 0, stream>>>(
-        le_h, text_h, inputs, att);
-    softmax512<<<B * L, 256, 0, stream>>>(att, att_h);
+    att_logits2<<<dim3(3, 64), 512, 0, stream>>>(
+        le_h, text_h, inputs, att_h);
     att_pv<<<dim3(3, 64), 512, 0, stream>>>(att_h, text_hT, feat_h);
     gemm_mfma<4, false, 2><<<dim3(2, 1, 141), 256, 0, stream>>>(
         feat_h, L * H, 0, out_Wh, L * H, 0, outacc, L, (long)B * L,
```

After: 439.3 us. -3.2%, faster.
